# Kernel optimization log

Measured on AMD Instinct MI355X. Metric: run time of the kernel, lower is better.

## Reference

```python
import jax, jax.numpy as jnp
import numpy as np

B, D, H = 4096, 2048, 2048

def setup_inputs() -> dict:
    key = jax.random.key(0)
    ks = jax.random.split(key, 16)
    s = 0.02  # small scale to keep tanh/sigmoid out of saturation
    inp = {
        'input_': jax.random.normal(ks[0], (B, D), jnp.float32),
        'h_prev': jax.random.normal(ks[1], (B, H), jnp.float32),
        'c_prev': jax.random.normal(ks[2], (B, H), jnp.float32),
        'w_xi': jax.random.normal(ks[3], (D, H), jnp.float32) * s,
        'w_hi': jax.random.normal(ks[4], (H, H), jnp.float32) * s,
        'w_ci': jax.random.normal(ks[5], (H, H), jnp.float32) * s,
        'w_xf': jax.random.normal(ks[6], (D, H), jnp.float32) * s,
        'w_hf': jax.random.normal(ks[7], (H, H), jnp.float32) * s,
        'w_cf': jax.random.normal(ks[8], (H, H), jnp.float32) * s,
        'w_xg': jax.random.normal(ks[9], (D, H), jnp.float32) * s,
        'w_hg': jax.random.normal(ks[10], (H, H), jnp.float32) * s,
        'w_xo': jax.random.normal(ks[11], (D, H), jnp.float32) * s,
        'w_ho': jax.random.normal(ks[12], (H, H), jnp.float32) * s,
        'w_co': jax.random.normal(ks[13], (H, H), jnp.float32) * s,
        'w_c':  jax.random.normal(ks[14], (H, H), jnp.float32) * s,
        'w_i':  jax.random.normal(ks[15], (D, H), jnp.float32) * s,
        'b_i': jnp.zeros((H,), jnp.float32),
        'b_f': jnp.zeros((H,), jnp.float32),
        'b_g': jnp.zeros((H,), jnp.float32),
        'b_o': jnp.zeros((H,), jnp.float32),
    }
    return inp

def reference(input_, h_prev, c_prev,
              w_xi, w_hi, w_ci, w_xf, w_hf, w_cf, w_xg, w_hg,
              w_xo, w_ho, w_co, w_c, w_i,
              b_i, b_f, b_g, b_o):
    # Fuse the x- and h-path GEMMs into concatenated matmuls (math-identical).
    wx = jnp.concatenate([w_xi, w_xf, w_xg, w_xo, w_i], axis=1)   # [D, 5H]
    wh = jnp.concatenate([w_hi, w_hf, w_hg, w_ho], axis=1)        # [H, 4H]
    wc = jnp.concatenate([w_ci, w_cf], axis=1)                    # [H, 2H]
    xz = input_ @ wx                                              # [B, 5H]
    hz = h_prev @ wh                                              # [B, 4H]
    cz = c_prev @ wc                                              # [B, 2H]
    Hd = w_hi.shape[0]
    i = xz[:, 0*Hd:1*Hd] + hz[:, 0*Hd:1*Hd] + cz[:, 0*Hd:1*Hd] + b_i
    f = xz[:, 1*Hd:2*Hd] + hz[:, 1*Hd:2*Hd] + cz[:, 1*Hd:2*Hd] + b_f
    g = xz[:, 2*Hd:3*Hd] + hz[:, 2*Hd:3*Hd] + b_g
    c = jax.nn.sigmoid(f) * c_prev + jax.nn.sigmoid(i) * jnp.tanh(g)
    o = xz[:, 3*Hd:4*Hd] + hz[:, 3*Hd:4*Hd] + c @ w_co + b_o
    h = jnp.tanh(o) * (jnp.tanh(c) @ w_c + xz[:, 4*Hd:5*Hd])
    return (h, c)
```

## Files before the change

kernel.cpp:

```cpp
#include <hip/hip_runtime.h>
#include <cstdint>
#include <cstddef>

typedef unsigned short u16;
typedef __bf16 bf16x8 __attribute__((ext_vector_type(8)));
typedef float f32x4 __attribute__((ext_vector_type(4)));
typedef u16 u16x8 __attribute__((ext_vector_type(8)));

#define B_DIM 4096
#define H_DIM 2048
#define BH 8388608

__device__ __forceinline__ float b2f(u16 x) {
  union { uint32_t u; float f; } v;
  v.u = ((uint32_t)x) << 16;
  return v.f;
}
__device__ __forceinline__ u16 f2b(float f) {
  union { float f; uint32_t u; } v;
  v.f = f;
  uint32_t r = v.u + 0x7FFFu + ((v.u >> 16) & 1u);
  return (u16)(r >> 16);
}
__device__ __forceinline__ float sigm(float x) { return 1.0f / (1.0f + __expf(-x)); }

typedef __attribute__((address_space(1))) void gv_t;
typedef __attribute__((address_space(3))) void lv_t;
__device__ __forceinline__ void g2lds16(const void* g, void* l) {
  __builtin_amdgcn_global_load_lds((gv_t*)g, (lv_t*)l, 16, 0, 0);
}

#define MFMA_BF16 __builtin_amdgcn_mfma_f32_16x16x32_bf16

struct CvtParams { const float* src[3]; u16* dst[3]; };

__global__ __launch_bounds__(256) void cvt_k(CvtParams p) {
  const float* __restrict__ s = p.src[blockIdx.y];
  u16* __restrict__ d = p.dst[blockIdx.y];
  size_t idx = ((size_t)blockIdx.x * 256 + threadIdx.x) * 8;
  float4 a = *(const float4*)(s + idx);
  float4 b = *(const float4*)(s + idx + 4);
  u16x8 o;
  o[0] = f2b(a.x); o[1] = f2b(a.y); o[2] = f2b(a.z); o[3] = f2b(a.w);
  o[4] = f2b(b.x); o[5] = f2b(b.y); o[6] = f2b(b.z); o[7] = f2b(b.w);
  *(u16x8*)(d + idx) = o;
}

struct TransParams {
  const float* src[13];
  u16* dst[13];
  int dstride[13];
};

__global__ __launch_bounds__(256) void transpose_k(TransParams p) {
  __shared__ u16 lds[64][72];
  const int mat = blockIdx.z;
  const float* __restrict__ src = p.src[mat];
  u16* __restrict__ dst = p.dst[mat];
  const int dstride = p.dstride[mat];
  const int tk = blockIdx.y * 64;
  const int tn = blockIdx.x * 64;
  const int t = threadIdx.x;
  const int lr = t >> 3;
  const int lc = (t & 7) * 8;
#pragma unroll
  for (int half = 0; half < 2; half++) {
    int r = lr + half * 32;
    const float4* g = (const float4*)(src + (size_t)(tk + r) * 2048 + tn + lc);
    float4 a = g[0], b = g[1];
    u16x8 t8;
    t8[0] = f2b(a.x); t8[1] = f2b(a.y); t8[2] = f2b(a.z); t8[3] = f2b(a.w);
    t8[4] = f2b(b.x); t8[5] = f2b(b.y); t8[6] = f2b(b.z); t8[7] = f2b(b.w);
    *(u16x8*)&lds[r][lc] = t8;
  }
  __syncthreads();
#pragma unroll
  for (int half = 0; half < 2; half++) {
    int n = lr + half * 32;
    u16x8 tmp;
#pragma unroll
    for (int j = 0; j < 8; j++) tmp[j] = lds[lc + j][n];
    *(u16x8*)(dst + (size_t)(tn + n) * dstride + tk + lc) = tmp;
  }
}

__device__ __forceinline__ void kloop256(
    const u16* __restrict__ A0, const u16* __restrict__ A1, const u16* __restrict__ A2,
    const u16* __restrict__ Wt, const int NT, const long Ktot,
    const int m0, const int n0,
    u16* lA0, u16* lA1, u16* lB0, u16* lB1,
    f32x4 (&acc)[8][4]) {
  const int tid = threadIdx.x;
  const int wave = tid >> 6, lane = tid & 63;
  const int fm = lane & 15, fkc = lane >> 4;
  const int x7 = fm & 7;
  const int wm = (wave >> 2) * 128, wn = (wave & 3) * 64;
  const int lr = tid >> 3;
  const int chunk = (tid & 7) ^ (lr & 7);
  const int stageOff = wave * 512;

  int raOff[8], rbOff[4];
#pragma unroll
  for (int i = 0; i < 8; i++) raOff[i] = (wm + i * 16 + fm) * 64;
#pragma unroll
  for (int j = 0; j < 4; j++) rbOff[j] = (wn + j * 16 + fm) * 64;
  const int so0 = ((fkc ^ x7) << 3);
  const int so1 = (((4 + fkc) ^ x7) << 3);

  auto stA = [&](int tt, int a, u16* dst) {
    const int seg = tt >> 5;
    const u16* base = (seg == 0) ? A0 : ((seg == 1) ? A1 : A2);
    const u16* src = base + (size_t)(m0 + a * 64 + lr) * 2048 + ((tt & 31) << 6) + (chunk << 3);
    g2lds16(src, dst + a * 4096 + stageOff);
  };
  auto stB = [&](int tt, int b, u16* dst) {
    const u16* src = Wt + (size_t)(n0 + b * 64 + lr) * Ktot + ((size_t)tt << 6) + (chunk << 3);
    g2lds16(src, dst + b * 4096 + stageOff);
  };

#pragma unroll
  for (int a = 0; a < 4; a++) stA(0, a, lA0);
#pragma unroll
  for (int b = 0; b < 4; b++) stB(0, b, lB0);
  const int t1c = (1 < NT) ? 1 : 0;
#pragma unroll
  for (int a = 0; a < 4; a++) stA(t1c, a, lA1);
  asm volatile("s_waitcnt vmcnt(4)" ::: "memory");
  __builtin_amdgcn_s_barrier();
  asm volatile("" ::: "memory");

  for (int t = 0; t < NT; ++t) {
    u16* lAp = (t & 1) ? lA1 : lA0;
    u16* lBp = (t & 1) ? lB1 : lB0;
    u16* lBq = (t & 1) ? lB0 : lB1;
    const int tn1 = (t + 1 < NT) ? t + 1 : NT - 1;
    const int tn2 = (t + 2 < NT) ? t + 2 : NT - 1;

    stB(tn1, 0, lBq);
    stB(tn1, 1, lBq);
    stB(tn1, 2, lBq);
    stB(tn1, 3, lBq);
    bf16x8 b01[2][2], a03[4][2], a47[4][2];
#pragma unroll
    for (int j = 0; j < 2; j++) {
      b01[j][0] = *(const bf16x8*)&lBp[rbOff[j] + so0];
      b01[j][1] = *(const bf16x8*)&lBp[rbOff[j] + so1];
    }
#pragma unroll
    for (int i = 0; i < 4; i++) {
      a03[i][0] = *(const bf16x8*)&lAp[raOff[i] + so0];
      a03[i][1] = *(const bf16x8*)&lAp[raOff[i] + so1];
    }
#pragma unroll
    for (int i = 0; i < 4; i++) {
      a47[i][0] = *(const bf16x8*)&lAp[raOff[4 + i] + so0];
      a47[i][1] = *(const bf16x8*)&lAp[raOff[4 + i] + so1];
    }
    __builtin_amdgcn_s_setprio(1);
#pragma unroll
    for (int ks = 0; ks < 2; ks++)
#pragma unroll
      for (int i = 0; i < 4; i++) {
        acc[i][0] = MFMA_BF16(a03[i][ks], b01[0][ks], acc[i][0], 0, 0, 0);
        acc[i][1] = MFMA_BF16(a03[i][ks], b01[1][ks], acc[i][1], 0, 0, 0);
      }
    __builtin_amdgcn_s_setprio(0);

    bf16x8 b23[2][2];
#pragma unroll
    for (int j = 0; j < 2; j++) {
      b23[j][0] = *(const bf16x8*)&lBp[rbOff[2 + j] + so0];
      b23[j][1] = *(const bf16x8*)&lBp[rbOff[2 + j] + so1];
    }
    __builtin_amdgcn_s_setprio(1);
#pragma unroll
    for (int ks = 0; ks < 2; ks++)
#pragma unroll
      for (int i = 0; i < 4; i++) {
        acc[4 + i][0] = MFMA_BF16(a47[i][ks], b01[0][ks], acc[4 + i][0], 0, 0, 0);
        acc[4 + i][1] = MFMA_BF16(a47[i][ks], b01[1][ks], acc[4 + i][1], 0, 0, 0);
      }
    __builtin_amdgcn_s_setprio(0);

    __builtin_amdgcn_s_barrier();
    asm volatile("" ::: "memory");

    stA(tn2, 0, lAp);
    stA(tn2, 1, lAp);
    __builtin_amdgcn_s_setprio(1);
#pragma unroll
    for (int ks = 0; ks < 2; ks++)
#pragma unroll
      for (int i = 0; i < 4; i++) {
        acc[i][2] = MFMA_BF16(a03[i][ks], b23[0][ks], acc[i][2], 0, 0, 0);
        acc[i][3] = MFMA_BF16(a03[i][ks], b23[1][ks], acc[i][3], 0, 0, 0);
      }
    __builtin_amdgcn_s_setprio(0);

    asm volatile("s_waitcnt vmcnt(2)" ::: "memory");
    __builtin_amdgcn_s_barrier();
    asm volatile("" ::: "memory");

    stA(tn2, 2, lAp);
    stA(tn2, 3, lAp);
    __builtin_amdgcn_s_setprio(1);
#pragma unroll
    for (int ks = 0; ks < 2; ks++)
#pragma unroll
      for (int i = 0; i < 4; i++) {
        acc[4 + i][2] = MFMA_BF16(a47[i][ks], b23[0][ks], acc[4 + i][2], 0, 0, 0);
        acc[4 + i][3] = MFMA_BF16(a47[i][ks], b23[1][ks], acc[4 + i][3], 0, 0, 0);
      }
    __builtin_amdgcn_s_setprio(0);
  }

  asm volatile("s_waitcnt vmcnt(0)" ::: "memory");
}

struct Gemm256Desc {
  const u16* A0; const u16* A1; const u16* A2;
  const u16* Wt; u16* C; int nseg;
};
struct Gemm256Params { Gemm256Desc d[5]; };

__global__ __launch_bounds__(512, 2) void gemm256_multi(Gemm256Params p) {
  const Gemm256Desc d = p.d[blockIdx.z];
  __shared__ u16 lA[2][16384];
  __shared__ u16 lB[2][16384];
  const int bid = blockIdx.y * 8 + blockIdx.x;
  const int swz = (bid & 7) * 16 + (bid >> 3);
  const int m0 = (swz >> 3) * 256, n0 = (swz & 7) * 256;
  const int NT = d.nseg << 5;
  const long Ktot = (long)NT << 6;

  f32x4 acc[8][4];
#pragma unroll
  for (int i = 0; i < 8; i++)
#pragma unroll
    for (int j = 0; j < 4; j++) acc[i][j] = (f32x4)0.0f;

  kloop256(d.A0, d.A1, d.A2, d.Wt, NT, Ktot, m0, n0, lA[0], lA[1], lB[0], lB[1], acc);

  const int lane = threadIdx.x & 63, wave = threadIdx.x >> 6;
  const int fm = lane & 15, quad = lane >> 4;
  const int wm = (wave >> 2) * 128, wn = (wave & 3) * 64;
#pragma unroll
  for (int i = 0; i < 8; i++)
#pragma unroll
    for (int j = 0; j < 4; j++)
#pragma unroll
      for (int r = 0; r < 4; r++) {
        size_t row = (size_t)(m0 + wm + i * 16 + quad * 4 + r);
        size_t col = (size_t)(n0 + wn + j * 16 + fm);
        d.C[row * 2048 + col] = f2b(acc[i][j][r]);
      }
}

struct GemmResParams {
  const u16* A[2]; const u16* W[2];
  u16* t1; float* t2;
};

__global__ __launch_bounds__(512, 2) void gemm256_res(GemmResParams p) {
  const int z = blockIdx.z;
  __shared__ u16 lA[2][16384];
  __shared__ u16 lB[2][16384];
  const int bid = blockIdx.y * 8 + blockIdx.x;
  const int swz = (bid & 7) * 16 + (bid >> 3);
  const int m0 = (swz >> 3) * 256, n0 = (swz & 7) * 256;

  f32x4 acc[8][4];
#pragma unroll
  for (int i = 0; i < 8; i++)
#pragma unroll
    for (int j = 0; j < 4; j++) acc[i][j] = (f32x4)0.0f;

  kloop256(p.A[z], nullptr, nullptr, p.W[z], 32, 2048, m0, n0, lA[0], lA[1], lB[0], lB[1], acc);

  const int lane = threadIdx.x & 63, wave = threadIdx.x >> 6;
  const int fm = lane & 15, quad = lane >> 4;
  const int wm = (wave >> 2) * 128, wn = (wave & 3) * 64;
  if (z == 0) {
#pragma unroll
    for (int i = 0; i < 8; i++)
#pragma unroll
      for (int j = 0; j < 4; j++)
#pragma unroll
        for (int r = 0; r < 4; r++) {
          size_t row = (size_t)(m0 + wm + i * 16 + quad * 4 + r);
          size_t col = (size_t)(n0 + wn + j * 16 + fm);
          p.t1[row * 2048 + col] = f2b(acc[i][j][r]);
        }
  } else {
#pragma unroll
    for (int i = 0; i < 8; i++)
#pragma unroll
      for (int j = 0; j < 4; j++)
#pragma unroll
        for (int r = 0; r < 4; r++) {
          size_t row = (size_t)(m0 + wm + i * 16 + quad * 4 + r);
          size_t col = (size_t)(n0 + wn + j * 16 + fm);
          p.t2[row * 2048 + col] = acc[i][j][r];
        }
  }
}

__global__ __launch_bounds__(256) void ew1_k(
    u16* __restrict__ zi, const u16* __restrict__ zf, u16* __restrict__ zg,
    const float* __restrict__ cprev, const float* __restrict__ bi,
    const float* __restrict__ bff, const float* __restrict__ bg,
    float* __restrict__ c_out) {
  size_t idx = ((size_t)blockIdx.x * 256 + threadIdx.x) * 8;
  int col = (int)(idx & (H_DIM - 1));
  u16x8 vzi = *(const u16x8*)(zi + idx);
  u16x8 vzf = *(const u16x8*)(zf + idx);
  u16x8 vzg = *(const u16x8*)(zg + idx);
  float4 cp0 = *(const float4*)(cprev + idx);
  float4 cp1 = *(const float4*)(cprev + idx + 4);
  float4 bi0 = *(const float4*)(bi + col), bi1 = *(const float4*)(bi + col + 4);
  float4 bf0 = *(const float4*)(bff + col), bf1 = *(const float4*)(bff + col + 4);
  float4 bg0 = *(const float4*)(bg + col), bg1 = *(const float4*)(bg + col + 4);
  float cpv[8] = {cp0.x, cp0.y, cp0.z, cp0.w, cp1.x, cp1.y, cp1.z, cp1.w};
  float biv[8] = {bi0.x, bi0.y, bi0.z, bi0.w, bi1.x, bi1.y, bi1.z, bi1.w};
  float bfv[8] = {bf0.x, bf0.y, bf0.z, bf0.w, bf1.x, bf1.y, bf1.z, bf1.w};
  float bgv[8] = {bg0.x, bg0.y, bg0.z, bg0.w, bg1.x, bg1.y, bg1.z, bg1.w};
  float cv[8], tcv[8];
#pragma unroll
  for (int e = 0; e < 8; e++) {
    float iv = b2f(vzi[e]) + biv[e];
    float fv = b2f(vzf[e]) + bfv[e];
    float gv = b2f(vzg[e]) + bgv[e];
    float c = sigm(fv) * cpv[e] + sigm(iv) * tanhf(gv);
    cv[e] = c;
    tcv[e] = tanhf(c);
  }
  u16x8 cb8, tc8;
#pragma unroll
  for (int e = 0; e < 8; e++) { cb8[e] = f2b(cv[e]); tc8[e] = f2b(tcv[e]); }
  *(u16x8*)(zi + idx) = cb8;
  *(u16x8*)(zg + idx) = tc8;
  float4 c0 = {cv[0], cv[1], cv[2], cv[3]}, c1 = {cv[4], cv[5], cv[6], cv[7]};
  *(float4*)(c_out + idx) = c0;
  *(float4*)(c_out + idx + 4) = c1;
}

__global__ __launch_bounds__(256) void ew2_k(
    const u16* __restrict__ zo, const u16* __restrict__ zr,
    const u16* __restrict__ t1, const float* __restrict__ t2,
    const float* __restrict__ bo, float* __restrict__ h) {
  size_t idx = ((size_t)blockIdx.x * 256 + threadIdx.x) * 8;
  int col = (int)(idx & (H_DIM - 1));
  u16x8 vo = *(const u16x8*)(zo + idx);
  u16x8 vr = *(const u16x8*)(zr + idx);
  u16x8 v1 = *(const u16x8*)(t1 + idx);
  float4 t2a = *(const float4*)(t2 + idx);
  float4 t2b = *(const float4*)(t2 + idx + 4);
  float4 bo0 = *(const float4*)(bo + col);
  float4 bo1 = *(const float4*)(bo + col + 4);
  float t2v[8] = {t2a.x, t2a.y, t2a.z, t2a.w, t2b.x, t2b.y, t2b.z, t2b.w};
  float bov[8] = {bo0.x, bo0.y, bo0.z, bo0.w, bo1.x, bo1.y, bo1.z, bo1.w};
  float hv[8];
#pragma unroll
  for (int e = 0; e < 8; e++) {
    float ov = b2f(vo[e]) + b2f(v1[e]) + bov[e];
    hv[e] = tanhf(ov) * (b2f(vr[e]) + t2v[e]);
  }
  float4 h0 = {hv[0], hv[1], hv[2], hv[3]}, h1 = {hv[4], hv[5], hv[6], hv[7]};
  *(float4*)(h + idx) = h0;
  *(float4*)(h + idx + 4) = h1;
}

extern "C" void kernel_launch(void* const* d_in, const int* in_sizes, int n_in,
                              void* d_out, int out_size, void* d_ws, size_t ws_size,
                              hipStream_t stream) {
  const float* input_ = (const float*)d_in[0];
  const float* h_prev = (const float*)d_in[1];
  const float* c_prev = (const float*)d_in[2];
  const float* w_xi = (const float*)d_in[3];
  const float* w_hi = (const float*)d_in[4];
  const float* w_ci = (const float*)d_in[5];
  const float* w_xf = (const float*)d_in[6];
  const float* w_hf = (const float*)d_in[7];
  const float* w_cf = (const float*)d_in[8];
  const float* w_xg = (const float*)d_in[9];
  const float* w_hg = (const float*)d_in[10];
  const float* w_xo = (const float*)d_in[11];
  const float* w_ho = (const float*)d_in[12];
  const float* w_co = (const float*)d_in[13];
  const float* w_c  = (const float*)d_in[14];
  const float* w_i  = (const float*)d_in[15];
  const float* b_i  = (const float*)d_in[16];
  const float* b_f  = (const float*)d_in[17];
  const float* b_g  = (const float*)d_in[18];
  const float* b_o  = (const float*)d_in[19];

  u16* ws = (u16*)d_ws;
  u16* WtI  = ws;
  u16* WtF  = WtI  + (size_t)2048 * 6144;
  u16* WtG  = WtF  + (size_t)2048 * 6144;
  u16* WtO  = WtG  + (size_t)2048 * 4096;
  u16* WtR  = WtO  + (size_t)2048 * 4096;
  u16* WtCO = WtR  + (size_t)2048 * 2048;
  u16* WtC  = WtCO + (size_t)2048 * 2048;
  u16* zi   = WtC  + (size_t)2048 * 2048;
  u16* zf   = zi + (size_t)BH;
  u16* zg   = zf + (size_t)BH;
  u16* zo   = zg + (size_t)BH;
  u16* zr   = zo + (size_t)BH;

  u16* t1buf = WtG;
  float* t2buf = (float*)WtI;

  u16* ob16 = (u16*)d_out;
  u16* xb = ob16;
  u16* hb = ob16 + (size_t)BH;
  u16* cb = ob16 + (size_t)2 * BH;
  float* out_f = (float*)d_out;
  float* h_out = out_f;
  float* c_out = out_f + (size_t)BH;

  CvtParams cp;
  cp.src[0] = input_; cp.src[1] = h_prev; cp.src[2] = c_prev;
  cp.dst[0] = xb; cp.dst[1] = hb; cp.dst[2] = cb;
  cvt_k<<<dim3(BH / 2048, 3), 256, 0, stream>>>(cp);

  TransParams tp;
  const float* srcs[13] = {w_xi, w_hi, w_ci, w_xf, w_hf, w_cf, w_xg, w_hg, w_xo, w_ho, w_i, w_co, w_c};
  u16* dsts[13] = {WtI, WtI + 2048, WtI + 4096, WtF, WtF + 2048, WtF + 4096,
                   WtG, WtG + 2048, WtO, WtO + 2048, WtR, WtCO, WtC};
  int strides[13] = {6144, 6144, 6144, 6144, 6144, 6144, 4096, 4096, 4096, 4096, 2048, 2048, 2048};
  for (int i = 0; i < 13; i++) { tp.src[i] = srcs[i]; tp.dst[i] = dsts[i]; tp.dstride[i] = strides[i]; }
  transpose_k<<<dim3(32, 32, 13), 256, 0, stream>>>(tp);

  Gemm256Params g1;
  g1.d[0] = {xb, hb, cb, WtI, zi, 3};
  g1.d[1] = {xb, hb, cb, WtF, zf, 3};
  g1.d[2] = {xb, hb, nullptr, WtG, zg, 2};
  g1.d[3] = {xb, hb, nullptr, WtO, zo, 2};
  g1.d[4] = {xb, nullptr, nullptr, WtR, zr, 1};
  gemm256_multi<<<dim3(8, 16, 5), 512, 0, stream>>>(g1);

  ew1_k<<<dim3(BH / 2048), 256, 0, stream>>>(zi, zf, zg, c_prev, b_i, b_f, b_g, c_out);

  GemmResParams gr;
  gr.A[0] = zi; gr.A[1] = zg; gr.W[0] = WtCO; gr.W[1] = WtC;
  gr.t1 = t1buf; gr.t2 = t2buf;
  gemm256_res<<<dim3(8, 16, 2), 512, 0, stream>>>(gr);

  ew2_k<<<dim3(BH / 2048), 256, 0, stream>>>(zo, zr, t1buf, t2buf, b_o, h_out);
}
```

Baseline: 811.1 us.

## Restructure GEMM k-loop into two-stage unrolled pipeline and split residual GEMM

Rewrites the shared k-loop as a template unrolled over two k-tiles, with explicit lgkmcnt/vmcnt waits and barriers that interleave LDS reads, global-to-LDS prefetches and MFMA groups more finely. It also moves the single-segment x@w_i GEMM out of the multi-GEMM launch into its own kernel that uses 256x128 tiles, giving 256 blocks instead of 128 for that work. The goal is better overlap of loads with MFMA and better load balance across CUs, since the short K=2048 GEMM no longer trails in the batched grid. The cost is many more barriers per iteration and an extra kernel launch.

```diff
diff --git a/kernel.cpp b/kernel.cpp
--- a/kernel.cpp
+++ b/kernel.cpp
@@ -31,6 +31,17 @@
 }
 
 #define MFMA_BF16 __builtin_amdgcn_mfma_f32_16x16x32_bf16
+
+#define FENCE asm volatile("" ::: "memory")
+#define BARRIER do { FENCE; __builtin_amdgcn_s_barrier(); FENCE; } while (0)
+#define LGKM0 do { asm volatile("s_waitcnt lgkmcnt(0)" ::: "memory"); \
+                   __builtin_amdgcn_sched_barrier(0); } while (0)
+#define LGKM8 asm volatile("s_waitcnt lgkmcnt(8)" ::: "memory")
+#define VMCNT2 asm volatile("s_waitcnt vmcnt(2)" ::: "memory")
+#define VMCNT4 asm volatile("s_waitcnt vmcnt(4)" ::: "memory")
+#define VMCNT0 asm volatile("s_waitcnt vmcnt(0)" ::: "memory")
+#define PRIO1 __builtin_amdgcn_s_setprio(1)
+#define PRIO0 __builtin_amdgcn_s_setprio(0)
 
 struct CvtParams { const float* src[3]; u16* dst[3]; };
 
@@ -84,144 +95,171 @@
   }
 }
 
-__device__ __forceinline__ void kloop256(
+template <int NF>
+__device__ __forceinline__ void kloop(
     const u16* __restrict__ A0, const u16* __restrict__ A1, const u16* __restrict__ A2,
     const u16* __restrict__ Wt, const int NT, const long Ktot,
     const int m0, const int n0,
     u16* lA0, u16* lA1, u16* lB0, u16* lB1,
-    f32x4 (&acc)[8][4]) {
+    f32x4 (&acc)[8][NF]) {
   const int tid = threadIdx.x;
   const int wave = tid >> 6, lane = tid & 63;
   const int fm = lane & 15, fkc = lane >> 4;
   const int x7 = fm & 7;
-  const int wm = (wave >> 2) * 128, wn = (wave & 3) * 64;
+  const int wm = (wave >> 2) * 128, wn = (wave & 3) * (NF * 16);
   const int lr = tid >> 3;
   const int chunk = (tid & 7) ^ (lr & 7);
   const int stageOff = wave * 512;
 
-  int raOff[8], rbOff[4];
+  int raOff[8], rbOff[NF];
 #pragma unroll
   for (int i = 0; i < 8; i++) raOff[i] = (wm + i * 16 + fm) * 64;
 #pragma unroll
-  for (int j = 0; j < 4; j++) rbOff[j] = (wn + j * 16 + fm) * 64;
+  for (int j = 0; j < NF; j++) rbOff[j] = (wn + j * 16 + fm) * 64;
   const int so0 = ((fkc ^ x7) << 3);
   const int so1 = (((4 + fkc) ^ x7) << 3);
 
-  auto stA = [&](int tt, int a, u16* dst) {
+  auto stA = [&](int tt, int r, u16* dstA) {
     const int seg = tt >> 5;
     const u16* base = (seg == 0) ? A0 : ((seg == 1) ? A1 : A2);
-    const u16* src = base + (size_t)(m0 + a * 64 + lr) * 2048 + ((tt & 31) << 6) + (chunk << 3);
-    g2lds16(src, dst + a * 4096 + stageOff);
+    g2lds16(base + (size_t)(m0 + r * 64 + lr) * 2048 + ((tt & 31) << 6) + (chunk << 3),
+            dstA + r * 4096 + stageOff);
   };
-  auto stB = [&](int tt, int b, u16* dst) {
-    const u16* src = Wt + (size_t)(n0 + b * 64 + lr) * Ktot + ((size_t)tt << 6) + (chunk << 3);
-    g2lds16(src, dst + b * 4096 + stageOff);
+  auto stB = [&](int tt, int r, u16* dstB) {
+    g2lds16(Wt + (size_t)(n0 + r * 64 + lr) * Ktot + ((size_t)tt << 6) + (chunk << 3),
+            dstB + r * 4096 + stageOff);
   };
-
-#pragma unroll
-  for (int a = 0; a < 4; a++) stA(0, a, lA0);
-#pragma unroll
-  for (int b = 0; b < 4; b++) stB(0, b, lB0);
-  const int t1c = (1 < NT) ? 1 : 0;
-#pragma unroll
-  for (int a = 0; a < 4; a++) stA(t1c, a, lA1);
-  asm volatile("s_waitcnt vmcnt(4)" ::: "memory");
-  __builtin_amdgcn_s_barrier();
-  asm volatile("" ::: "memory");
-
-  for (int t = 0; t < NT; ++t) {
-    u16* lAp = (t & 1) ? lA1 : lA0;
-    u16* lBp = (t & 1) ? lB1 : lB0;
-    u16* lBq = (t & 1) ? lB0 : lB1;
-    const int tn1 = (t + 1 < NT) ? t + 1 : NT - 1;
-    const int tn2 = (t + 2 < NT) ? t + 2 : NT - 1;
-
-    stB(tn1, 0, lBq);
-    stB(tn1, 1, lBq);
-    stB(tn1, 2, lBq);
-    stB(tn1, 3, lBq);
-    bf16x8 b01[2][2], a03[4][2], a47[4][2];
+  auto rdA = [&](const u16* l, bf16x8 (&d)[4][2], int base) {
+#pragma unroll
+    for (int i = 0; i < 4; i++) {
+      d[i][0] = *(const bf16x8*)&l[raOff[base + i] + so0];
+      d[i][1] = *(const bf16x8*)&l[raOff[base + i] + so1];
+    }
+  };
+  auto rdB = [&](const u16* l, bf16x8 (&d)[2][2], int base) {
 #pragma unroll
     for (int j = 0; j < 2; j++) {
-      b01[j][0] = *(const bf16x8*)&lBp[rbOff[j] + so0];
-      b01[j][1] = *(const bf16x8*)&lBp[rbOff[j] + so1];
+      d[j][0] = *(const bf16x8*)&l[rbOff[base + j] + so0];
+      d[j][1] = *(const bf16x8*)&l[rbOff[base + j] + so1];
     }
-#pragma unroll
-    for (int i = 0; i < 4; i++) {
-      a03[i][0] = *(const bf16x8*)&lAp[raOff[i] + so0];
-      a03[i][1] = *(const bf16x8*)&lAp[raOff[i] + so1];
+  };
+  auto mfma16 = [&](bf16x8 (&a)[4][2], bf16x8 (&b)[2][2], int mi, int nj) {
+#pragma unroll
+    for (int ks = 0; ks < 2; ks++)
+#pragma unroll
+      for (int i = 0; i < 4; i++) {
+        acc[mi + i][nj + 0] = MFMA_BF16(a[i][ks], b[0][ks], acc[mi + i][nj + 0], 0, 0, 0);
+        acc[mi + i][nj + 1] = MFMA_BF16(a[i][ks], b[1][ks], acc[mi + i][nj + 1], 0, 0, 0);
+      }
+  };
+
+  const int NI = NT >> 1;
+  bf16x8 a03[4][2], a47[4][2], b01[2][2], b23[2][2];
+
+  if constexpr (NF == 4) {
+#pragma unroll
+    for (int r = 0; r < 4; r++) stA(0, r, lA0);
+#pragma unroll
+    for (int r = 0; r < 4; r++) stB(0, r, lB0);
+#pragma unroll
+    for (int r = 0; r < 4; r++) stA(1, r, lA1);
+    VMCNT4;
+    BARRIER;
+
+    for (int it = 0; it < NI; ++it) {
+      const int tE = 2 * it, tO = 2 * it + 1;
+      const int tE2 = (tE + 2 < NT) ? tE + 2 : NT - 1;
+      const int tO2 = (tO + 2 < NT) ? tO + 2 : NT - 1;
+      rdA(lA0, a03, 0); rdB(lB0, b01, 0);
+      stB(tO, 0, lB1); stB(tO, 1, lB1);
+      LGKM8;
+      BARRIER; LGKM0;
+      PRIO1; mfma16(a03, b01, 0, 0); PRIO0;
+      BARRIER;
+      rdA(lA0, a47, 4);
+      stB(tO, 2, lB1); stB(tO, 3, lB1);
+      BARRIER; LGKM0;
+      PRIO1; mfma16(a47, b01, 4, 0); PRIO0;
+      BARRIER;
+      rdB(lB0, b23, 2);
+      stA(tE2, 0, lA0); stA(tE2, 1, lA0);
+      BARRIER; LGKM0;
+      PRIO1; mfma16(a03, b23, 0, 2); PRIO0;
+      BARRIER;
+      stA(tE2, 2, lA0); stA(tE2, 3, lA0);
+      BARRIER;
+      PRIO1; mfma16(a47, b23, 4, 2); PRIO0;
+      VMCNT4;
+      BARRIER;
+      rdA(lA1, a03, 0); rdB(lB1, b01, 0);
+      stB(tE2, 0, lB0); stB(tE2, 1, lB0);
+      LGKM8;
+      BARRIER; LGKM0;
+      PRIO1; mfma16(a03, b01, 0, 0); PRIO0;
+      BARRIER;
+      rdA(lA1, a47, 4);
+      stB(tE2, 2, lB0); stB(tE2, 3, lB0);
+      BARRIER; LGKM0;
+      PRIO1; mfma16(a47, b01, 4, 0); PRIO0;
+      BARRIER;
+      rdB(lB1, b23, 2);
+      stA(tO2, 0, lA1); stA(tO2, 1, lA1);
+      BARRIER; LGKM0;
+      PRIO1; mfma16(a03, b23, 0, 2); PRIO0;
+      BARRIER;
+      stA(tO2, 2, lA1); stA(tO2, 3, lA1);
+      BARRIER;
+      PRIO1; mfma16(a47, b23, 4, 2); PRIO0;
+      VMCNT4;
+      BARRIER;
     }
-#pragma unroll
-    for (int i = 0; i < 4; i++) {
-      a47[i][0] = *(const bf16x8*)&lAp[raOff[4 + i] + so0];
-      a47[i][1] = *(const bf16x8*)&lAp[raOff[4 + i] + so1];
+  } else {
+#pragma unroll
+    for (int r = 0; r < 4; r++) stA(0, r, lA0);
+    stB(0, 0, lB0); stB(0, 1, lB0);
+    stB(1, 0, lB1); stB(1, 1, lB1);
+    VMCNT2;
+    BARRIER;
+
+    for (int it = 0; it < NI; ++it) {
+      const int tE = 2 * it, tO = 2 * it + 1;
+      const int tE2 = (tE + 2 < NT) ? tE + 2 : NT - 1;
+      const int tO2 = (tO + 2 < NT) ? tO + 2 : NT - 1;
+      rdA(lA0, a03, 0); rdB(lB0, b01, 0);
+      stA(tO, 0, lA1); stA(tO, 1, lA1); stA(tO, 2, lA1); stA(tO, 3, lA1);
+      LGKM8;
+      BARRIER; LGKM0;
+      PRIO1; mfma16(a03, b01, 0, 0); PRIO0;
+      BARRIER;
+      rdA(lA0, a47, 4);
+      stB(tE2, 0, lB0); stB(tE2, 1, lB0);
+      BARRIER; LGKM0;
+      PRIO1; mfma16(a47, b01, 4, 0); PRIO0;
+      VMCNT2;
+      BARRIER;
+      rdA(lA1, a03, 0); rdB(lB1, b01, 0);
+      stA(tE2, 0, lA0); stA(tE2, 1, lA0); stA(tE2, 2, lA0); stA(tE2, 3, lA0);
+      LGKM8;
+      BARRIER; LGKM0;
+      PRIO1; mfma16(a03, b01, 0, 0); PRIO0;
+      BARRIER;
+      rdA(lA1, a47, 4);
+      stB(tO2, 0, lB1); stB(tO2, 1, lB1);
+      BARRIER; LGKM0;
+      PRIO1; mfma16(a47, b01, 4, 0); PRIO0;
+      VMCNT2;
+      BARRIER;
     }
-    __builtin_amdgcn_s_setprio(1);
-#pragma unroll
-    for (int ks = 0; ks < 2; ks++)
-#pragma unroll
-      for (int i = 0; i < 4; i++) {
-        acc[i][0] = MFMA_BF16(a03[i][ks], b01[0][ks], acc[i][0], 0, 0, 0);
-        acc[i][1] = MFMA_BF16(a03[i][ks], b01[1][ks], acc[i][1], 0, 0, 0);
-      }
-    __builtin_amdgcn_s_setprio(0);
-
-    bf16x8 b23[2][2];
-#pragma unroll
-    for (int j = 0; j < 2; j++) {
-      b23[j][0] = *(const bf16x8*)&lBp[rbOff[2 + j] + so0];
-      b23[j][1] = *(const bf16x8*)&lBp[rbOff[2 + j] + so1];
-    }
-    __builtin_amdgcn_s_setprio(1);
-#pragma unroll
-    for (int ks = 0; ks < 2; ks++)
-#pragma unroll
-      for (int i = 0; i < 4; i++) {
-        acc[4 + i][0] = MFMA_BF16(a47[i][ks], b01[0][ks], acc[4 + i][0], 0, 0, 0);
-        acc[4 + i][1] = MFMA_BF16(a47[i][ks], b01[1][ks], acc[4 + i][1], 0, 0, 0);
-      }
-    __builtin_amdgcn_s_setprio(0);
-
-    __builtin_amdgcn_s_barrier();
-    asm volatile("" ::: "memory");
-
-    stA(tn2, 0, lAp);
-    stA(tn2, 1, lAp);
-    __builtin_amdgcn_s_setprio(1);
-#pragma unroll
-    for (int ks = 0; ks < 2; ks++)
-#pragma unroll
-      for (int i = 0; i < 4; i++) {
-        acc[i][2] = MFMA_BF16(a03[i][ks], b23[0][ks], acc[i][2], 0, 0, 0);
-        acc[i][3] = MFMA_BF16(a03[i][ks], b23[1][ks], acc[i][3], 0, 0, 0);
-      }
-    __builtin_amdgcn_s_setprio(0);
-
-    asm volatile("s_waitcnt vmcnt(2)" ::: "memory");
-    __builtin_amdgcn_s_barrier();
-    asm volatile("" ::: "memory");
-
-    stA(tn2, 2, lAp);
-    stA(tn2, 3, lAp);
-    __builtin_amdgcn_s_setprio(1);
-#pragma unroll
-    for (int ks = 0; ks < 2; ks++)
-#pragma unroll
-      for (int i = 0; i < 4; i++) {
-        acc[4 + i][2] = MFMA_BF16(a47[i][ks], b23[0][ks], acc[4 + i][2], 0, 0, 0);
-        acc[4 + i][3] = MFMA_BF16(a47[i][ks], b23[1][ks], acc[4 + i][3], 0, 0, 0);
-      }
-    __builtin_amdgcn_s_setprio(0);
   }
 
-  asm volatile("s_waitcnt vmcnt(0)" ::: "memory");
+  VMCNT0;
 }
 
 struct Gemm256Desc {
   const u16* A0; const u16* A1; const u16* A2;
   const u16* Wt; u16* C; int nseg;
 };
-struct Gemm256Params { Gemm256Desc d[5]; };
+struct Gemm256Params { Gemm256Desc d[4]; };
 
 __global__ __launch_bounds__(512, 2) void gemm256_multi(Gemm256Params p) {
   const Gemm256Desc d = p.d[blockIdx.z];
@@ -239,7 +277,7 @@
 #pragma unroll
     for (int j = 0; j < 4; j++) acc[i][j] = (f32x4)0.0f;
 
-  kloop256(d.A0, d.A1, d.A2, d.Wt, NT, Ktot, m0, n0, lA[0], lA[1], lB[0], lB[1], acc);
+  kloop<4>(d.A0, d.A1, d.A2, d.Wt, NT, Ktot, m0, n0, lA[0], lA[1], lB[0], lB[1], acc);
 
   const int lane = threadIdx.x & 63, wave = threadIdx.x >> 6;
   const int fm = lane & 15, quad = lane >> 4;
@@ -253,6 +291,37 @@
         size_t row = (size_t)(m0 + wm + i * 16 + quad * 4 + r);
         size_t col = (size_t)(n0 + wn + j * 16 + fm);
         d.C[row * 2048 + col] = f2b(acc[i][j][r]);
+      }
+}
+
+__global__ __launch_bounds__(512, 2) void gemm_r(
+    const u16* __restrict__ A, const u16* __restrict__ Wt, u16* __restrict__ C) {
+  __shared__ u16 lA[2][16384];
+  __shared__ u16 lB[2][8192];
+  const int bid = blockIdx.x;
+  const int swz = (bid & 7) * 32 + (bid >> 3);
+  const int m0 = (swz >> 4) * 256, n0 = (swz & 15) * 128;
+
+  f32x4 acc[8][2];
+#pragma unroll
+  for (int i = 0; i < 8; i++)
+#pragma unroll
+    for (int j = 0; j < 2; j++) acc[i][j] = (f32x4)0.0f;
+
+  kloop<2>(A, nullptr, nullptr, Wt, 32, 2048, m0, n0, lA[0], lA[1], lB[0], lB[1], acc);
+
+  const int lane = threadIdx.x & 63, wave = threadIdx.x >> 6;
+  const int fm = lane & 15, quad = lane >> 4;
+  const int wm = (wave >> 2) * 128, wn = (wave & 3) * 32;
+#pragma unroll
+  for (int i = 0; i < 8; i++)
+#pragma unroll
+    for (int j = 0; j < 2; j++)
+#pragma unroll
+      for (int r = 0; r < 4; r++) {
+        size_t row = (size_t)(m0 + wm + i * 16 + quad * 4 + r);
+        size_t col = (size_t)(n0 + wn + j * 16 + fm);
+        C[row * 2048 + col] = f2b(acc[i][j][r]);
       }
 }
 
@@ -275,7 +344,7 @@
 #pragma unroll
     for (int j = 0; j < 4; j++) acc[i][j] = (f32x4)0.0f;
 
-  kloop256(p.A[z], nullptr, nullptr, p.W[z], 32, 2048, m0, n0, lA[0], lA[1], lB[0], lB[1], acc);
+  kloop<4>(p.A[z], nullptr, nullptr, p.W[z], 32, 2048, m0, n0, lA[0], lA[1], lB[0], lB[1], acc);
 
   const int lane = threadIdx.x & 63, wave = threadIdx.x >> 6;
   const int fm = lane & 15, quad = lane >> 4;
@@ -437,8 +506,9 @@
   g1.d[1] = {xb, hb, cb, WtF, zf, 3};
   g1.d[2] = {xb, hb, nullptr, WtG, zg, 2};
   g1.d[3] = {xb, hb, nullptr, WtO, zo, 2};
-  g1.d[4] = {xb, nullptr, nullptr, WtR, zr, 1};
-  gemm256_multi<<<dim3(8, 16, 5), 512, 0, stream>>>(g1);
+  gemm256_multi<<<dim3(8, 16, 4), 512, 0, stream>>>(g1);
+
+  gemm_r<<<dim3(256), 512, 0, stream>>>(xb, WtR, zr);
 
   ew1_k<<<dim3(BH / 2048), 256, 0, stream>>>(zi, zf, zg, c_prev, b_i, b_f, b_g, c_out);
 
```

Measured after the change: 813.4 us. About the same (+0.3%).

## Shrink GEMM tiles to 128x128 and load B fragments directly from global memory

Applied to the files above, without the earlier changes.

Replaces the 256x256, 512-thread GEMM main loop with a 128x128, 256-thread variant that stages only A in LDS and reads the transposed weight fragments directly from global memory into registers. This is meant to cut LDS footprint and register pressure so three blocks fit per CU, and to simplify the barrier schedule. In exchange, B operands lose LDS reuse and depend on L2/global latency every k-step, the per-block arithmetic intensity drops, and the grid block swizzle is removed.

```diff
diff --git a/kernel.cpp b/kernel.cpp
--- a/kernel.cpp
+++ b/kernel.cpp
@@ -31,6 +31,13 @@
 }
 
 #define MFMA_BF16 __builtin_amdgcn_mfma_f32_16x16x32_bf16
+
+#define FENCE asm volatile("" ::: "memory")
+#define BARRIER do { FENCE; __builtin_amdgcn_s_barrier(); FENCE; } while (0)
+#define VMCNT4 asm volatile("s_waitcnt vmcnt(4)" ::: "memory")
+#define VMCNT0 asm volatile("s_waitcnt vmcnt(0)" ::: "memory")
+#define PRIO1 __builtin_amdgcn_s_setprio(1)
+#define PRIO0 __builtin_amdgcn_s_setprio(0)
 
 struct CvtParams { const float* src[3]; u16* dst[3]; };
 
@@ -84,168 +91,111 @@
   }
 }
 
-__device__ __forceinline__ void kloop256(
+__device__ __forceinline__ void kloop128bd(
     const u16* __restrict__ A0, const u16* __restrict__ A1, const u16* __restrict__ A2,
     const u16* __restrict__ Wt, const int NT, const long Ktot,
     const int m0, const int n0,
-    u16* lA0, u16* lA1, u16* lB0, u16* lB1,
-    f32x4 (&acc)[8][4]) {
+    u16* lA0, u16* lA1,
+    f32x4 (&acc)[4][4]) {
   const int tid = threadIdx.x;
   const int wave = tid >> 6, lane = tid & 63;
   const int fm = lane & 15, fkc = lane >> 4;
   const int x7 = fm & 7;
-  const int wm = (wave >> 2) * 128, wn = (wave & 3) * 64;
-  const int lr = tid >> 3;
-  const int chunk = (tid & 7) ^ (lr & 7);
+  const int wm = (wave >> 1) * 64, wn = (wave & 1) * 64;
+  const int srow = tid >> 3;
+  const int schunk = (tid & 7) ^ (srow & 7);
   const int stageOff = wave * 512;
 
-  int raOff[8], rbOff[4];
-#pragma unroll
-  for (int i = 0; i < 8; i++) raOff[i] = (wm + i * 16 + fm) * 64;
-#pragma unroll
-  for (int j = 0; j < 4; j++) rbOff[j] = (wn + j * 16 + fm) * 64;
+  int raOff[4];
+#pragma unroll
+  for (int i = 0; i < 4; i++) raOff[i] = (wm + i * 16 + fm) * 64;
   const int so0 = ((fkc ^ x7) << 3);
   const int so1 = (((4 + fkc) ^ x7) << 3);
 
-  auto stA = [&](int tt, int a, u16* dst) {
+  const u16* pB[4];
+#pragma unroll
+  for (int j = 0; j < 4; j++)
+    pB[j] = Wt + (size_t)(n0 + wn + j * 16 + fm) * Ktot + (fkc << 3);
+
+  auto stageA = [&](int tt, u16* buf) {
     const int seg = tt >> 5;
     const u16* base = (seg == 0) ? A0 : ((seg == 1) ? A1 : A2);
-    const u16* src = base + (size_t)(m0 + a * 64 + lr) * 2048 + ((tt & 31) << 6) + (chunk << 3);
-    g2lds16(src, dst + a * 4096 + stageOff);
+    const u16* srcB = base + ((size_t)(tt & 31) << 6) + (schunk << 3);
+#pragma unroll
+    for (int r = 0; r < 4; r++)
+      g2lds16(srcB + (size_t)(m0 + r * 32 + srow) * 2048, buf + r * 2048 + stageOff);
   };
-  auto stB = [&](int tt, int b, u16* dst) {
-    const u16* src = Wt + (size_t)(n0 + b * 64 + lr) * Ktot + ((size_t)tt << 6) + (chunk << 3);
-    g2lds16(src, dst + b * 4096 + stageOff);
-  };
-
-#pragma unroll
-  for (int a = 0; a < 4; a++) stA(0, a, lA0);
-#pragma unroll
-  for (int b = 0; b < 4; b++) stB(0, b, lB0);
-  const int t1c = (1 < NT) ? 1 : 0;
-#pragma unroll
-  for (int a = 0; a < 4; a++) stA(t1c, a, lA1);
-  asm volatile("s_waitcnt vmcnt(4)" ::: "memory");
-  __builtin_amdgcn_s_barrier();
-  asm volatile("" ::: "memory");
+
+  stageA(0, lA0);
+  stageA((1 < NT) ? 1 : 0, lA1);
+  VMCNT4;
+  BARRIER;
 
   for (int t = 0; t < NT; ++t) {
-    u16* lAp = (t & 1) ? lA1 : lA0;
-    u16* lBp = (t & 1) ? lB1 : lB0;
-    u16* lBq = (t & 1) ? lB0 : lB1;
-    const int tn1 = (t + 1 < NT) ? t + 1 : NT - 1;
+    u16* bufp = (t & 1) ? lA1 : lA0;
+
+    bf16x8 b[2][4];
+#pragma unroll
+    for (int ks = 0; ks < 2; ks++)
+#pragma unroll
+      for (int j = 0; j < 4; j++)
+        b[ks][j] = *(const bf16x8*)(pB[j] + ((size_t)t << 6) + (ks << 5));
+
+    bf16x8 a[4][2];
+#pragma unroll
+    for (int i = 0; i < 4; i++) {
+      a[i][0] = *(const bf16x8*)&bufp[raOff[i] + so0];
+      a[i][1] = *(const bf16x8*)&bufp[raOff[i] + so1];
+    }
+
+    BARRIER;
+
     const int tn2 = (t + 2 < NT) ? t + 2 : NT - 1;
-
-    stB(tn1, 0, lBq);
-    stB(tn1, 1, lBq);
-    stB(tn1, 2, lBq);
-    stB(tn1, 3, lBq);
-    bf16x8 b01[2][2], a03[4][2], a47[4][2];
-#pragma unroll
-    for (int j = 0; j < 2; j++) {
-      b01[j][0] = *(const bf16x8*)&lBp[rbOff[j] + so0];
-      b01[j][1] = *(const bf16x8*)&lBp[rbOff[j] + so1];
-    }
-#pragma unroll
-    for (int i = 0; i < 4; i++) {
-      a03[i][0] = *(const bf16x8*)&lAp[raOff[i] + so0];
-      a03[i][1] = *(const bf16x8*)&lAp[raOff[i] + so1];
-    }
-#pragma unroll
-    for (int i = 0; i < 4; i++) {
-      a47[i][0] = *(const bf16x8*)&lAp[raOff[4 + i] + so0];
-      a47[i][1] = *(const bf16x8*)&lAp[raOff[4 + i] + so1];
-    }
-    __builtin_amdgcn_s_setprio(1);
+    stageA(tn2, bufp);
+
+    VMCNT4;
+    BARRIER;
+
+    PRIO1;
 #pragma unroll
     for (int ks = 0; ks < 2; ks++)
 #pragma unroll
-      for (int i = 0; i < 4; i++) {
-        acc[i][0] = MFMA_BF16(a03[i][ks], b01[0][ks], acc[i][0], 0, 0, 0);
-        acc[i][1] = MFMA_BF16(a03[i][ks], b01[1][ks], acc[i][1], 0, 0, 0);
-      }
-    __builtin_amdgcn_s_setprio(0);
-
-    bf16x8 b23[2][2];
-#pragma unroll
-    for (int j = 0; j < 2; j++) {
-      b23[j][0] = *(const bf16x8*)&lBp[rbOff[2 + j] + so0];
-      b23[j][1] = *(const bf16x8*)&lBp[rbOff[2 + j] + so1];
-    }
-    __builtin_amdgcn_s_setprio(1);
-#pragma unroll
-    for (int ks = 0; ks < 2; ks++)
-#pragma unroll
-      for (int i = 0; i < 4; i++) {
-        acc[4 + i][0] = MFMA_BF16(a47[i][ks], b01[0][ks], acc[4 + i][0], 0, 0, 0);
-        acc[4 + i][1] = MFMA_BF16(a47[i][ks], b01[1][ks], acc[4 + i][1], 0, 0, 0);
-      }
-    __builtin_amdgcn_s_setprio(0);
-
-    __builtin_amdgcn_s_barrier();
-    asm volatile("" ::: "memory");
-
-    stA(tn2, 0, lAp);
-    stA(tn2, 1, lAp);
-    __builtin_amdgcn_s_setprio(1);
-#pragma unroll
-    for (int ks = 0; ks < 2; ks++)
-#pragma unroll
-      for (int i = 0; i < 4; i++) {
-        acc[i][2] = MFMA_BF16(a03[i][ks], b23[0][ks], acc[i][2], 0, 0, 0);
-        acc[i][3] = MFMA_BF16(a03[i][ks], b23[1][ks], acc[i][3], 0, 0, 0);
-      }
-    __builtin_amdgcn_s_setprio(0);
-
-    asm volatile("s_waitcnt vmcnt(2)" ::: "memory");
-    __builtin_amdgcn_s_barrier();
-    asm volatile("" ::: "memory");
-
-    stA(tn2, 2, lAp);
-    stA(tn2, 3, lAp);
-    __builtin_amdgcn_s_setprio(1);
-#pragma unroll
-    for (int ks = 0; ks < 2; ks++)
-#pragma unroll
-      for (int i = 0; i < 4; i++) {
-        acc[4 + i][2] = MFMA_BF16(a47[i][ks], b23[0][ks], acc[4 + i][2], 0, 0, 0);
-        acc[4 + i][3] = MFMA_BF16(a47[i][ks], b23[1][ks], acc[4 + i][3], 0, 0, 0);
-      }
-    __builtin_amdgcn_s_setprio(0);
-  }
-
-  asm volatile("s_waitcnt vmcnt(0)" ::: "memory");
-}
-
-struct Gemm256Desc {
+      for (int i = 0; i < 4; i++)
+#pragma unroll
+        for (int j = 0; j < 4; j++)
+          acc[i][j] = MFMA_BF16(a[i][ks], b[ks][j], acc[i][j], 0, 0, 0);
+    PRIO0;
+  }
+
+  VMCNT0;
+}
+
+struct GemmDesc {
   const u16* A0; const u16* A1; const u16* A2;
   const u16* Wt; u16* C; int nseg;
 };
-struct Gemm256Params { Gemm256Desc d[5]; };
-
-__global__ __launch_bounds__(512, 2) void gemm256_multi(Gemm256Params p) {
-  const Gemm256Desc d = p.d[blockIdx.z];
-  __shared__ u16 lA[2][16384];
-  __shared__ u16 lB[2][16384];
-  const int bid = blockIdx.y * 8 + blockIdx.x;
-  const int swz = (bid & 7) * 16 + (bid >> 3);
-  const int m0 = (swz >> 3) * 256, n0 = (swz & 7) * 256;
+struct GemmParams { GemmDesc d[5]; };
+
+__global__ __launch_bounds__(256, 3) void gemm_multi(GemmParams p) {
+  const GemmDesc d = p.d[blockIdx.z];
+  __shared__ u16 lA[2][8192];
+  const int m0 = blockIdx.y * 128, n0 = blockIdx.x * 128;
   const int NT = d.nseg << 5;
   const long Ktot = (long)NT << 6;
 
-  f32x4 acc[8][4];
-#pragma unroll
-  for (int i = 0; i < 8; i++)
+  f32x4 acc[4][4];
+#pragma unroll
+  for (int i = 0; i < 4; i++)
 #pragma unroll
     for (int j = 0; j < 4; j++) acc[i][j] = (f32x4)0.0f;
 
-  kloop256(d.A0, d.A1, d.A2, d.Wt, NT, Ktot, m0, n0, lA[0], lA[1], lB[0], lB[1], acc);
+  kloop128bd(d.A0, d.A1, d.A2, d.Wt, NT, Ktot, m0, n0, lA[0], lA[1], acc);
 
   const int lane = threadIdx.x & 63, wave = threadIdx.x >> 6;
   const int fm = lane & 15, quad = lane >> 4;
-  const int wm = (wave >> 2) * 128, wn = (wave & 3) * 64;
-#pragma unroll
-  for (int i = 0; i < 8; i++)
+  const int wm = (wave >> 1) * 64, wn = (wave & 1) * 64;
+#pragma unroll
+  for (int i = 0; i < 4; i++)
 #pragma unroll
     for (int j = 0; j < 4; j++)
 #pragma unroll
@@ -261,28 +211,25 @@
   u16* t1; float* t2;
 };
 
-__global__ __launch_bounds__(512, 2) void gemm256_res(GemmResParams p) {
+__global__ __launch_bounds__(256, 3) void gemm_res(GemmResParams p) {
   const int z = blockIdx.z;
-  __shared__ u16 lA[2][16384];
-  __shared__ u16 lB[2][16384];
-  const int bid = blockIdx.y * 8 + blockIdx.x;
-  const int swz = (bid & 7) * 16 + (bid >> 3);
-  const int m0 = (swz >> 3) * 256, n0 = (swz & 7) * 256;
-
-  f32x4 acc[8][4];
-#pragma unroll
-  for (int i = 0; i < 8; i++)
+  __shared__ u16 lA[2][8192];
+  const int m0 = blockIdx.y * 128, n0 = blockIdx.x * 128;
+
+  f32x4 acc[4][4];
+#pragma unroll
+  for (int i = 0; i < 4; i++)
 #pragma unroll
     for (int j = 0; j < 4; j++) acc[i][j] = (f32x4)0.0f;
 
-  kloop256(p.A[z], nullptr, nullptr, p.W[z], 32, 2048, m0, n0, lA[0], lA[1], lB[0], lB[1], acc);
+  kloop128bd(p.A[z], nullptr, nullptr, p.W[z], 32, 2048, m0, n0, lA[0], lA[1], acc);
 
   const int lane = threadIdx.x & 63, wave = threadIdx.x >> 6;
   const int fm = lane & 15, quad = lane >> 4;
-  const int wm = (wave >> 2) * 128, wn = (wave & 3) * 64;
+  const int wm = (wave >> 1) * 64, wn = (wave & 1) * 64;
   if (z == 0) {
 #pragma unroll
-    for (int i = 0; i < 8; i++)
+    for (int i = 0; i < 4; i++)
 #pragma unroll
       for (int j = 0; j < 4; j++)
 #pragma unroll
@@ -293,7 +240,7 @@
         }
   } else {
 #pragma unroll
-    for (int i = 0; i < 8; i++)
+    for (int i = 0; i < 4; i++)
 #pragma unroll
       for (int j = 0; j < 4; j++)
 #pragma unroll
@@ -432,20 +379,20 @@
   for (int i = 0; i < 13; i++) { tp.src[i] = srcs[i]; tp.dst[i] = dsts[i]; tp.dstride[i] = strides[i]; }
   transpose_k<<<dim3(32, 32, 13), 256, 0, stream>>>(tp);
 
-  Gemm256Params g1;
+  GemmParams g1;
   g1.d[0] = {xb, hb, cb, WtI, zi, 3};
   g1.d[1] = {xb, hb, cb, WtF, zf, 3};
   g1.d[2] = {xb, hb, nullptr, WtG, zg, 2};
   g1.d[3] = {xb, hb, nullptr, WtO, zo, 2};
   g1.d[4] = {xb, nullptr, nullptr, WtR, zr, 1};
-  gemm256_multi<<<dim3(8, 16, 5), 512, 0, stream>>>(g1);
+  gemm_multi<<<dim3(16, 32, 5), 256, 0, stream>>>(g1);
 
   ew1_k<<<dim3(BH / 2048), 256, 0, stream>>>(zi, zf, zg, c_prev, b_i, b_f, b_g, c_out);
 
   GemmResParams gr;
   gr.A[0] = zi; gr.A[1] = zg; gr.W[0] = WtCO; gr.W[1] = WtC;
   gr.t1 = t1buf; gr.t2 = t2buf;
-  gemm256_res<<<dim3(8, 16, 2), 512, 0, stream>>>(gr);
+  gemm_res<<<dim3(16, 32, 2), 256, 0, stream>>>(gr);
 
   ew2_k<<<dim3(BH / 2048), 256, 0, stream>>>(zo, zr, t1buf, t2buf, b_o, h_out);
 }
```

After: 1.259 ms. 1.55x slower.
